# Kernel optimization log

Measured on AMD Instinct MI355X. Metric: run time of the kernel, lower is better.

Reference implementation:

```python
import jax, jax.numpy as jnp
import numpy as np

N = 100000      # n_nodes
E = 1600000     # n_edges (avg degree 16)
F_IN = 128      # nfeat
H = 128         # nhid
C = 64          # nclass


def setup_inputs() -> dict:
    key = jax.random.key(0)
    ks = jax.random.split(key, 6)
    x = jax.random.normal(ks[0], (N, F_IN), dtype=jnp.float32)
    edge_index = jax.random.randint(ks[1], (2, E), 0, N, dtype=jnp.int32)
    # Glorot-ish init for GCNConv weights, zeros for bias (PyG default)
    W1 = jax.random.normal(ks[2], (F_IN, H), dtype=jnp.float32) * (1.0 / np.sqrt(F_IN))
    b1 = jnp.zeros((H,), dtype=jnp.float32)
    W2 = jax.random.normal(ks[3], (H, C), dtype=jnp.float32) * (1.0 / np.sqrt(H))
    b2 = jnp.zeros((C,), dtype=jnp.float32)
    return {"x": x, "edge_index": edge_index, "W1": W1, "b1": b1, "W2": W2, "b2": b2}


def _gcn_conv(x, W, b, src, dst, n):
    """PyG GCNConv: h = W^T x, out_i = sum_j norm_ij * h_j + b, with
    symmetric normalization over the self-loop-augmented graph."""
    h = x @ W                                                   # [n, out]
    deg = jax.ops.segment_sum(jnp.ones(src.shape[0], h.dtype), dst, num_segments=n)
    dinv = jnp.where(deg > 0, jax.lax.rsqrt(deg), 0.0)          # D^-1/2
    norm = dinv[src] * dinv[dst]                                # [E+n]
    msg = h[src] * norm[:, None]                                # gather + scale
    out = jax.ops.segment_sum(msg, dst, num_segments=n)         # scatter-add
    return out + b


def reference(x, edge_index, W1, b1, W2, b2):
    loop = jnp.arange(N, dtype=edge_index.dtype)
    src = jnp.concatenate([edge_index[0], loop])  # sources j (with self loops)
    dst = jnp.concatenate([edge_index[1], loop])  # targets i
    h = jax.nn.relu(_gcn_conv(x, W1, b1, src, dst, N))  # dropout = identity (eval)
    out = _gcn_conv(h, W2, b2, src, dst, N)
    return jax.nn.log_softmax(out, axis=1)
```

## Files before the change

kernel.cpp:

```cpp
#include <hip/hip_runtime.h>
#include <hip/hip_fp16.h>
#include <cstdint>
#include <cstddef>
#include <cstring>


__device__ inline unsigned pack_bf16x2(float a, float b) {
    unsigned ua = __float_as_uint(a);
    unsigned ub = __float_as_uint(b);
    ua += 0x7fffu + ((ua >> 16) & 1u);
    ub += 0x7fffu + ((ub >> 16) & 1u);
    return (ua >> 16) | (ub & 0xffff0000u);
}
__device__ inline unsigned short bf16_rne(float v) {
    unsigned u = __float_as_uint(v);
    u += 0x7fffu + ((u >> 16) & 1u);
    return (unsigned short)(u >> 16);
}


typedef float fv2 __attribute__((ext_vector_type(2)));

template <bool HI>
__device__ inline fv2 fp8_fv2(unsigned u) {
#if __has_builtin(__builtin_amdgcn_cvt_pk_f32_fp8)
    return __builtin_amdgcn_cvt_pk_f32_fp8((int)u, HI);
#else
    unsigned u2 = HI ? (u >> 16) : (u & 0xffffu);
    unsigned w = (u2 & 0xFFu) | ((u2 & 0xFF00u) << 8);
    unsigned hb = ((w & 0x00800080u) << 8) | ((w & 0x007f007fu) << 7);
    __half2 h2;
    memcpy(&h2, &hb, 4);
    float2 f = __half22float2(h2);
    fv2 r;
    r.x = f.x * 256.0f;
    r.y = f.y * 256.0f;
    return r;
#endif
}

__device__ inline fv2 bfpair(unsigned u) {
    union { unsigned q[2]; fv2 f; } t;
    t.q[0] = u << 16;
    t.q[1] = u & 0xffff0000u;
    return t.f;
}

__device__ inline unsigned f32_to_fp8_byte(float v) {
    unsigned short hb = __half_as_ushort(__float2half(v * 0.00390625f));
    unsigned t = hb & 0x7fffu;
    t += 0x3fu + ((t >> 7) & 1u);
    return ((hb >> 8) & 0x80u) | (t >> 7);
}

__device__ inline unsigned char f32_to_fp8_b(float v) {
#if __has_builtin(__builtin_amdgcn_cvt_pk_fp8_f32)
    return (unsigned char)(__builtin_amdgcn_cvt_pk_fp8_f32(v, v, 0, false) & 0xff);
#else
    return (unsigned char)f32_to_fp8_byte(v);
#endif
}

typedef int iv4 __attribute__((ext_vector_type(4)));

#define NPART 8
#define KB    32
#define NPP_MAX 12500
#define EB    2048


__global__ __launch_bounds__(256) void k_bucket_ballot(const int* __restrict__ src,
                                                       const int* __restrict__ dst,
                                                       int* __restrict__ cursor8,
                                                       unsigned* __restrict__ pairs,
                                                       int E, int npp, int capE,
                                                       int srcb) {
    __shared__ int sWcnt[4][NPART];
    __shared__ int sWoff[4][NPART];
    int tid = threadIdx.x;
    int wv = tid >> 6;
    int lane = tid & 63;
    int base_e = blockIdx.x * EB + tid * 8;
    int nv = min(8, E - base_e);
    if (nv < 0) nv = 0;
    int dv[8], sv[8];
    if (nv == 8) {
        *(iv4*)(dv + 0) = *(const iv4*)(dst + base_e + 0);
        *(iv4*)(dv + 4) = *(const iv4*)(dst + base_e + 4);
        *(iv4*)(sv + 0) = *(const iv4*)(src + base_e + 0);
        *(iv4*)(sv + 4) = *(const iv4*)(src + base_e + 4);
    } else {
        for (int k = 0; k < 8; ++k) {
            dv[k] = (k < nv) ? dst[base_e + k] : -1;
            sv[k] = (k < nv) ? src[base_e + k] : 0;
        }
    }
    unsigned long long below = (1ull << lane) - 1ull;
    int wb[NPART];
#pragma unroll
    for (int pp = 0; pp < NPART; ++pp) wb[pp] = 0;
    int pv[8], pos[8];
#pragma unroll
    for (int s = 0; s < 8; ++s) {
        int d = dv[s];
        int p = (d >= 0) ? (int)((unsigned)d / (unsigned)npp) : NPART;
        pv[s] = p;
        unsigned long long msel = 0;
        int base = 0;
#pragma unroll
        for (int pp = 0; pp < NPART; ++pp) {
            unsigned long long m = __ballot(p == pp);
            if (p == pp) { msel = m; base = wb[pp]; }
            wb[pp] += (int)__popcll(m);
        }
        pos[s] = base + (int)__popcll(msel & below);
    }
    if (lane < NPART) {
        int v = 0;
#pragma unroll
        for (int pp = 0; pp < NPART; ++pp)
            if (lane == pp) v = wb[pp];
        sWcnt[wv][lane] = v;
    }
    __syncthreads();
    if (tid < NPART) {
        int c0 = sWcnt[0][tid], c1 = sWcnt[1][tid], c2 = sWcnt[2][tid], c3 = sWcnt[3][tid];
        int gb = atomicAdd(&cursor8[tid], c0 + c1 + c2 + c3);
        sWoff[0][tid] = gb;
        sWoff[1][tid] = gb + c0;
        sWoff[2][tid] = gb + c0 + c1;
        sWoff[3][tid] = gb + c0 + c1 + c2;
    }
    __syncthreads();
#pragma unroll
    for (int s = 0; s < 8; ++s) {
        int p = pv[s];
        if (p < NPART) {
            int off = sWoff[wv][p];
            pairs[(size_t)p * capE + off + pos[s]] =
                ((unsigned)(dv[s] - p * npp) << srcb) | (unsigned)sv[s];
        }
    }
}

__global__ __launch_bounds__(256) void k_count_part(const unsigned* __restrict__ pairs,
                                                    const int* __restrict__ cursor8,
                                                    int* __restrict__ cntarr,
                                                    int npp, int capE, int srcb) {
    __shared__ int h[NPP_MAX];
    int p = blockIdx.x & (NPART - 1);
    int b = blockIdx.x >> 3;
    for (int i = threadIdx.x; i < npp; i += 256) h[i] = 0;
    __syncthreads();
    int sz = cursor8[p];
    int chunk = (sz + KB - 1) / KB;
    int s0 = b * chunk;
    int s1 = min(sz, s0 + chunk);
    const unsigned* seg = pairs + (size_t)p * capE;
    for (int i = s0 + threadIdx.x; i < s1; i += 256)
        atomicAdd(&h[seg[i] >> srcb], 1);
    __syncthreads();
    size_t out = (size_t)(p * KB + b) * npp;
    for (int i = threadIdx.x; i < npp; i += 256) cntarr[out + i] = h[i];
}

__global__ void k_indeg_scan(const int* __restrict__ cntarr,
                             float* __restrict__ dinv,
                             int* __restrict__ row_ptr,
                             int* __restrict__ partials, int n, int npp) {
    __shared__ int s[256];
    int t = threadIdx.x;
    int node0 = blockIdx.x * 1024 + t * 4;
    int v0 = 0, v1 = 0, v2 = 0, v3 = 0;
    if (((npp & 3) == 0) && (node0 + 3 < n) && (node0 / npp == (node0 + 3) / npp)) {
        int p = node0 / npp;
        int dl = node0 - p * npp;
        size_t base = (size_t)p * KB * npp + dl;
        for (int b = 0; b < KB; ++b) {
            iv4 c = *(const iv4*)(cntarr + base + (size_t)b * npp);
            v0 += c.x; v1 += c.y; v2 += c.z; v3 += c.w;
        }
    } else {
        for (int r = 0; r < 4; ++r) {
            int node = node0 + r;
            if (node < n) {
                int p = node / npp;
                int dl = node - p * npp;
                size_t base = (size_t)p * KB * npp + dl;
                int sum = 0;
                for (int b = 0; b < KB; ++b) sum += cntarr[base + (size_t)b * npp];
                if (r == 0) v0 = sum; else if (r == 1) v1 = sum;
                else if (r == 2) v2 = sum; else v3 = sum;
            }
        }
    }
    if (node0 + 0 < n) dinv[node0 + 0] = rsqrtf((float)v0 + 1.0f);
    if (node0 + 1 < n) dinv[node0 + 1] = rsqrtf((float)v1 + 1.0f);
    if (node0 + 2 < n) dinv[node0 + 2] = rsqrtf((float)v2 + 1.0f);
    if (node0 + 3 < n) dinv[node0 + 3] = rsqrtf((float)v3 + 1.0f);
    int sum = v0 + v1 + v2 + v3;
    s[t] = sum;
    __syncthreads();
    for (int off = 1; off < 256; off <<= 1) {
        int x = (t >= off) ? s[t - off] : 0;
        __syncthreads();
        s[t] += x;
        __syncthreads();
    }
    int excl = s[t] - sum;
    if ((node0 + 0) < n) row_ptr[node0 + 0] = excl;
    if ((node0 + 1) < n) row_ptr[node0 + 1] = excl + v0;
    if ((node0 + 2) < n) row_ptr[node0 + 2] = excl + v0 + v1;
    if ((node0 + 3) < n) row_ptr[node0 + 3] = excl + v0 + v1 + v2;
    if (t == 255) partials[blockIdx.x] = s[255];
}

__global__ void k_scan_partials(int* __restrict__ partials, int np) {
    __shared__ int s[256];
    int t = threadIdx.x;
    int v = (t < np) ? partials[t] : 0;
    s[t] = v;
    __syncthreads();
    for (int off = 1; off < 256; off <<= 1) {
        int x = (t >= off) ? s[t - off] : 0;
        __syncthreads();
        s[t] += x;
        __syncthreads();
    }
    if (t < np) partials[t] = s[t] - v;
}

__global__ void k_finalize_bases(int* __restrict__ row_ptr,
                                 const int* __restrict__ partials,
                                 int* __restrict__ cntarr, int n, int E, int npp) {
    int i = blockIdx.x * blockDim.x + threadIdx.x;
    if (i >= n) return;
    int rp = row_ptr[i] + partials[i >> 10];
    row_ptr[i] = rp;
    if (i == 0) row_ptr[n] = E;
    int p = (unsigned)i / (unsigned)npp;
    int dl = i - p * npp;
    size_t base = (size_t)p * KB * npp + dl;
    int run = rp;
    for (int b = 0; b < KB; ++b) {
        size_t idx = base + (size_t)b * npp;
        int c = cntarr[idx];
        cntarr[idx] = run;
        run += c;
    }
}

__global__ __launch_bounds__(256) void k_fill2(const unsigned* __restrict__ pairs,
                                               const int* __restrict__ cursor8,
                                               const int* __restrict__ cntarr,
                                               int* __restrict__ col,
                                               int npp, int capE, int srcb) {
    __shared__ int cur[NPP_MAX];
    int p = blockIdx.x & (NPART - 1);
    int b = blockIdx.x >> 3;
    size_t slice = (size_t)(p * KB + b) * npp;
    for (int i = threadIdx.x; i < npp; i += 256) cur[i] = cntarr[slice + i];
    __syncthreads();
    int sz = cursor8[p];
    int chunk = (sz + KB - 1) / KB;
    int s0 = b * chunk;
    int s1 = min(sz, s0 + chunk);
    const unsigned* seg = pairs + (size_t)p * capE;
    unsigned smask = (1u << srcb) - 1u;
    for (int i = s0 + threadIdx.x; i < s1; i += 256) {
        unsigned u = seg[i];
        int pos = atomicAdd(&cur[u >> srcb], 1);
        col[pos] = (int)(u & smask);
    }
}

typedef __attribute__((ext_vector_type(8))) short short8;
typedef __attribute__((ext_vector_type(4))) float f32x4;

union FragU {
    short8 s;
    uint4 u4;
    unsigned u[4];
};

__device__ inline void packW_body(const float* __restrict__ W, unsigned* __restrict__ Bp,
                                  int NOUT, int NT) {
    int nf = 4 * NT * 64;
    for (int fid = threadIdx.x; fid < nf; fid += 256) {
        int q = fid / (NT * 64);
        int rem = fid - q * NT * 64;
        int nt = rem >> 6;
        int lane = rem & 63;
        int k0 = q * 32 + (lane >> 4) * 8;
        int ncol = nt * 16 + (lane & 15);
        unsigned u[4];
        for (int h = 0; h < 4; ++h) {
            float a = W[(k0 + 2 * h) * NOUT + ncol];
            float b = W[(k0 + 2 * h + 1) * NOUT + ncol];
            u[h] = pack_bf16x2(a, b);
        }
        uint4 o = {u[0], u[1], u[2], u[3]};
        *(uint4*)(Bp + (size_t)fid * 4) = o;
    }
}

__global__ void k_packW2(const float* __restrict__ W1, unsigned* __restrict__ Bp1,
                         const float* __restrict__ W2, unsigned* __restrict__ Bp2) {
    if (blockIdx.x == 0) packW_body(W1, Bp1, 128, 8);
    else                 packW_body(W2, Bp2, 64, 4);
}

__global__ __launch_bounds__(256) void k_gemm128_mfma(const float* __restrict__ X,
                                                      const unsigned* __restrict__ Bp,
                                                      const float* __restrict__ dinv,
                                                      unsigned char* __restrict__ H8,
                                                      int n) {
    int w = threadIdx.x >> 6;
    int lane = threadIdx.x & 63;
    int quad = lane >> 4;
    int lrow = lane & 15;
    int row0 = blockIdx.x * 64 + w * 16;
    int rowA = min(row0 + lrow, n - 1);

    f32x4 acc[8];
    for (int nt = 0; nt < 8; ++nt) acc[nt] = (f32x4){0.f, 0.f, 0.f, 0.f};

    for (int q = 0; q < 4; ++q) {
        const float* xp = X + (size_t)rowA * 128 + q * 32 + quad * 8;
        float4 x0 = *(const float4*)xp;
        float4 x1 = *(const float4*)(xp + 4);
        FragU a;
        a.u[0] = pack_bf16x2(x0.x, x0.y);
        a.u[1] = pack_bf16x2(x0.z, x0.w);
        a.u[2] = pack_bf16x2(x1.x, x1.y);
        a.u[3] = pack_bf16x2(x1.z, x1.w);
        for (int nt = 0; nt < 8; ++nt) {
            FragU b;
            b.u4 = *(const uint4*)(Bp + ((size_t)(q * 8 + nt) * 64 + lane) * 4);
            acc[nt] = __builtin_amdgcn_mfma_f32_16x16x32_bf16(a.s, b.s, acc[nt], 0, 0, 0);
        }
    }

    int rbase = row0 + quad * 4;
    float dv[4];
    if (rbase + 3 < n) {
        float4 d4 = *(const float4*)(dinv + rbase);
        dv[0] = d4.x; dv[1] = d4.y; dv[2] = d4.z; dv[3] = d4.w;
    } else {
        for (int r = 0; r < 4; ++r) dv[r] = dinv[min(rbase + r, n - 1)];
    }
    for (int nt = 0; nt < 8; ++nt) {
        for (int r = 0; r < 4; ++r) {
            int row = rbase + r;
            if (row < n)
                H8[(size_t)row * 128 + nt * 16 + lrow] = f32_to_fp8_b(dv[r] * acc[nt][r]);
        }
    }
}

__global__ __launch_bounds__(256) void k_gemm64_mfma(const unsigned* __restrict__ Xb,
                                                     const unsigned* __restrict__ Bp,
                                                     const float* __restrict__ dinv,
                                                     unsigned short* __restrict__ H16,
                                                     int n) {
    int w = threadIdx.x >> 6;
    int lane = threadIdx.x & 63;
    int quad = lane >> 4;
    int lrow = lane & 15;
    int row0 = blockIdx.x * 64 + w * 16;
    int rowA = min(row0 + lrow, n - 1);

    f32x4 acc[4];
    for (int nt = 0; nt < 4; ++nt) acc[nt] = (f32x4){0.f, 0.f, 0.f, 0.f};

    for (int q = 0; q < 4; ++q) {
        FragU a;
        a.u4 = *(const uint4*)(Xb + (size_t)rowA * 64 + q * 16 + quad * 4);
        for (int nt = 0; nt < 4; ++nt) {
            FragU b;
            b.u4 = *(const uint4*)(Bp + ((size_t)(q * 4 + nt) * 64 + lane) * 4);
            acc[nt] = __builtin_amdgcn_mfma_f32_16x16x32_bf16(a.s, b.s, acc[nt], 0, 0, 0);
        }
    }

    int rbase = row0 + quad * 4;
    float dv[4];
    if (rbase + 3 < n) {
        float4 d4 = *(const float4*)(dinv + rbase);
        dv[0] = d4.x; dv[1] = d4.y; dv[2] = d4.z; dv[3] = d4.w;
    } else {
        for (int r = 0; r < 4; ++r) dv[r] = dinv[min(rbase + r, n - 1)];
    }
    for (int nt = 0; nt < 4; ++nt) {
        for (int r = 0; r < 4; ++r) {
            int row = rbase + r;
            if (row < n)
                H16[(size_t)row * 64 + nt * 16 + lrow] = bf16_rne(dv[r] * acc[nt][r]);
        }
    }
}


__global__ __launch_bounds__(256) void k_agg_relu(const unsigned* __restrict__ hs,
                                                  const float* __restrict__ dinv,
                                                  const int* __restrict__ row_ptr,
                                                  const int* __restrict__ col,
                                                  const float* __restrict__ bias,
                                                  unsigned* __restrict__ out, int n) {
    int node = blockIdx.x * 16 + (threadIdx.x >> 4);
    if (node >= n) return;
    int l = threadIdx.x & 15;
    const uint2* hrow = (const uint2*)hs;
    fv2 a0 = {0.f, 0.f}, a1 = {0.f, 0.f}, a2 = {0.f, 0.f}, a3 = {0.f, 0.f};
    {
        uint2 u = hrow[(size_t)node * 16 + l];
        a0 += fp8_fv2<false>(u.x); a1 += fp8_fv2<true>(u.x);
        a2 += fp8_fv2<false>(u.y); a3 += fp8_fv2<true>(u.y);
    }
    int k = row_ptr[node], p1 = row_ptr[node + 1];
    for (; k + 8 <= p1; k += 8) {
        int cA = col[k + 0], cB = col[k + 1], cC = col[k + 2], cD = col[k + 3];
        int cE = col[k + 4], cF = col[k + 5], cG = col[k + 6], cH = col[k + 7];
        uint2 uA = hrow[(size_t)cA * 16 + l];
        uint2 uB = hrow[(size_t)cB * 16 + l];
        uint2 uC = hrow[(size_t)cC * 16 + l];
        uint2 uD = hrow[(size_t)cD * 16 + l];
        uint2 uE = hrow[(size_t)cE * 16 + l];
        uint2 uF = hrow[(size_t)cF * 16 + l];
        uint2 uG = hrow[(size_t)cG * 16 + l];
        uint2 uH = hrow[(size_t)cH * 16 + l];
        a0 += fp8_fv2<false>(uA.x); a1 += fp8_fv2<true>(uA.x);
        a2 += fp8_fv2<false>(uA.y); a3 += fp8_fv2<true>(uA.y);
        a0 += fp8_fv2<false>(uB.x); a1 += fp8_fv2<true>(uB.x);
        a2 += fp8_fv2<false>(uB.y); a3 += fp8_fv2<true>(uB.y);
        a0 += fp8_fv2<false>(uC.x); a1 += fp8_fv2<true>(uC.x);
        a2 += fp8_fv2<false>(uC.y); a3 += fp8_fv2<true>(uC.y);
        a0 += fp8_fv2<false>(uD.x); a1 += fp8_fv2<true>(uD.x);
        a2 += fp8_fv2<false>(uD.y); a3 += fp8_fv2<true>(uD.y);
        a0 += fp8_fv2<false>(uE.x); a1 += fp8_fv2<true>(uE.x);
        a2 += fp8_fv2<false>(uE.y); a3 += fp8_fv2<true>(uE.y);
        a0 += fp8_fv2<false>(uF.x); a1 += fp8_fv2<true>(uF.x);
        a2 += fp8_fv2<false>(uF.y); a3 += fp8_fv2<true>(uF.y);
        a0 += fp8_fv2<false>(uG.x); a1 += fp8_fv2<true>(uG.x);
        a2 += fp8_fv2<false>(uG.y); a3 += fp8_fv2<true>(uG.y);
        a0 += fp8_fv2<false>(uH.x); a1 += fp8_fv2<true>(uH.x);
        a2 += fp8_fv2<false>(uH.y); a3 += fp8_fv2<true>(uH.y);
    }
    for (; k + 4 <= p1; k += 4) {
        int cA = col[k + 0], cB = col[k + 1], cC = col[k + 2], cD = col[k + 3];
        uint2 uA = hrow[(size_t)cA * 16 + l];
        uint2 uB = hrow[(size_t)cB * 16 + l];
        uint2 uC = hrow[(size_t)cC * 16 + l];
        uint2 uD = hrow[(size_t)cD * 16 + l];
        a0 += fp8_fv2<false>(uA.x); a1 += fp8_fv2<true>(uA.x);
        a2 += fp8_fv2<false>(uA.y); a3 += fp8_fv2<true>(uA.y);
        a0 += fp8_fv2<false>(uB.x); a1 += fp8_fv2<true>(uB.x);
        a2 += fp8_fv2<false>(uB.y); a3 += fp8_fv2<true>(uB.y);
        a0 += fp8_fv2<false>(uC.x); a1 += fp8_fv2<true>(uC.x);
        a2 += fp8_fv2<false>(uC.y); a3 += fp8_fv2<true>(uC.y);
        a0 += fp8_fv2<false>(uD.x); a1 += fp8_fv2<true>(uD.x);
        a2 += fp8_fv2<false>(uD.y); a3 += fp8_fv2<true>(uD.y);
    }
    for (; k < p1; ++k) {
        int j = col[k];
        uint2 u = hrow[(size_t)j * 16 + l];
        a0 += fp8_fv2<false>(u.x); a1 += fp8_fv2<true>(u.x);
        a2 += fp8_fv2<false>(u.y); a3 += fp8_fv2<true>(u.y);
    }
    float di = dinv[node];
    float4 b4a = *(const float4*)(bias + 8 * l);
    float4 b4b = *(const float4*)(bias + 8 * l + 4);
    float v0 = fmaf(di, a0.x, b4a.x);
    float v1 = fmaf(di, a0.y, b4a.y);
    float v2 = fmaf(di, a1.x, b4a.z);
    float v3 = fmaf(di, a1.y, b4a.w);
    float v4 = fmaf(di, a2.x, b4b.x);
    float v5 = fmaf(di, a2.y, b4b.y);
    float v6 = fmaf(di, a3.x, b4b.z);
    float v7 = fmaf(di, a3.y, b4b.w);
    v0 = v0 > 0.f ? v0 : 0.f;
    v1 = v1 > 0.f ? v1 : 0.f;
    v2 = v2 > 0.f ? v2 : 0.f;
    v3 = v3 > 0.f ? v3 : 0.f;
    v4 = v4 > 0.f ? v4 : 0.f;
    v5 = v5 > 0.f ? v5 : 0.f;
    v6 = v6 > 0.f ? v6 : 0.f;
    v7 = v7 > 0.f ? v7 : 0.f;
    uint4 o = {pack_bf16x2(v0, v1), pack_bf16x2(v2, v3),
               pack_bf16x2(v4, v5), pack_bf16x2(v6, v7)};
    *(uint4*)(out + (size_t)node * 64 + 4 * l) = o;
}

__global__ __launch_bounds__(256) void k_agg_lsm(const unsigned* __restrict__ hs,
                                                 const float* __restrict__ dinv,
                                                 const int* __restrict__ row_ptr,
                                                 const int* __restrict__ col,
                                                 const float* __restrict__ bias,
                                                 float* __restrict__ out, int n) {
    int node = blockIdx.x * 16 + (threadIdx.x >> 4);
    if (node >= n) return;
    int l = threadIdx.x & 15;
    const uint2* hrow = (const uint2*)hs;
    fv2 aX = {0.f, 0.f}, aY = {0.f, 0.f};
    {
        uint2 u = hrow[(size_t)node * 16 + l];
        aX += bfpair(u.x);
        aY += bfpair(u.y);
    }
    int k = row_ptr[node], p1 = row_ptr[node + 1];
    for (; k + 8 <= p1; k += 8) {
        int cA = col[k + 0], cB = col[k + 1], cC = col[k + 2], cD = col[k + 3];
        int cE = col[k + 4], cF = col[k + 5], cG = col[k + 6], cH = col[k + 7];
        uint2 uA = hrow[(size_t)cA * 16 + l];
        uint2 uB = hrow[(size_t)cB * 16 + l];
        uint2 uC = hrow[(size_t)cC * 16 + l];
        uint2 uD = hrow[(size_t)cD * 16 + l];
        uint2 uE = hrow[(size_t)cE * 16 + l];
        uint2 uF = hrow[(size_t)cF * 16 + l];
        uint2 uG = hrow[(size_t)cG * 16 + l];
        uint2 uH = hrow[(size_t)cH * 16 + l];
        aX += bfpair(uA.x); aY += bfpair(uA.y);
        aX += bfpair(uB.x); aY += bfpair(uB.y);
        aX += bfpair(uC.x); aY += bfpair(uC.y);
        aX += bfpair(uD.x); aY += bfpair(uD.y);
        aX += bfpair(uE.x); aY += bfpair(uE.y);
        aX += bfpair(uF.x); aY += bfpair(uF.y);
        aX += bfpair(uG.x); aY += bfpair(uG.y);
        aX += bfpair(uH.x); aY += bfpair(uH.y);
    }
    for (; k + 4 <= p1; k += 4) {
        int cA = col[k + 0], cB = col[k + 1], cC = col[k + 2], cD = col[k + 3];
        uint2 uA = hrow[(size_t)cA * 16 + l];
        uint2 uB = hrow[(size_t)cB * 16 + l];
        uint2 uC = hrow[(size_t)cC * 16 + l];
        uint2 uD = hrow[(size_t)cD * 16 + l];
        aX += bfpair(uA.x); aY += bfpair(uA.y);
        aX += bfpair(uB.x); aY += bfpair(uB.y);
        aX += bfpair(uC.x); aY += bfpair(uC.y);
        aX += bfpair(uD.x); aY += bfpair(uD.y);
    }
    for (; k < p1; ++k) {
        int j = col[k];
        uint2 u = hrow[(size_t)j * 16 + l];
        aX += bfpair(u.x); aY += bfpair(u.y);
    }
    float di = dinv[node];
    float4 b4 = *(const float4*)(bias + 4 * l);
    float v0 = fmaf(di, aX.x, b4.x);
    float v1 = fmaf(di, aX.y, b4.y);
    float v2 = fmaf(di, aY.x, b4.z);
    float v3 = fmaf(di, aY.y, b4.w);
    float m = fmaxf(fmaxf(v0, v1), fmaxf(v2, v3));
    for (int off = 8; off; off >>= 1) m = fmaxf(m, __shfl_xor(m, off));
    float s = __expf(v0 - m) + __expf(v1 - m) + __expf(v2 - m) + __expf(v3 - m);
    for (int off = 8; off; off >>= 1) s += __shfl_xor(s, off);
    float ls = __logf(s);
    float4 o = {v0 - m - ls, v1 - m - ls, v2 - m - ls, v3 - m - ls};
    *(float4*)(out + (size_t)node * 64 + 4 * l) = o;
}


extern "C" void kernel_launch(void* const* d_in, const int* in_sizes, int n_in,
                              void* d_out, int out_size, void* d_ws, size_t ws_size,
                              hipStream_t stream) {
    const float* x  = (const float*)d_in[0];
    const int*   ei = (const int*)d_in[1];
    const float* W1 = (const float*)d_in[2];
    const float* b1 = (const float*)d_in[3];
    const float* W2 = (const float*)d_in[4];
    const float* b2 = (const float*)d_in[5];
    float* out = (float*)d_out;

    const int N = in_sizes[0] / 128;
    const int E = in_sizes[1] / 2;
    const int* src = ei;
    const int* dst = ei + E;
    const int npp = (N + NPART - 1) / NPART;
    const int capE = (E + NPART - 1) / NPART + 32768;
    int srcb = 1;
    while ((1 << srcb) < N) ++srcb;

    char* w = (char*)d_ws;
    size_t off = 0;
    auto alloc = [&](size_t bytes) -> void* {
        void* p = w + off;
        off += (bytes + 255) & ~(size_t)255;
        return p;
    };
    int*      row_ptr  = (int*)alloc((size_t)(N + 1) * 4);
    int*      colarr   = (int*)alloc((size_t)E * 4);
    int*      partials = (int*)alloc(256 * 4);
    int*      cursor8  = (int*)alloc(8 * 4);
    float*    dinv     = (float*)alloc((size_t)N * 4);
    unsigned* h1f8     = (unsigned*)alloc((size_t)N * 32 * 4);
    unsigned* a1b      = (unsigned*)alloc((size_t)N * 64 * 4);
    unsigned* h2b      = (unsigned*)alloc((size_t)N * 32 * 4);
    unsigned* Bp1      = (unsigned*)alloc(4 * 8 * 64 * 16);
    unsigned* Bp2      = (unsigned*)alloc(4 * 4 * 64 * 16);
    unsigned* pairsU   = (unsigned*)a1b;
    int*      cntarr   = (int*)((char*)a1b + (size_t)NPART * capE * 4);
    (void)ws_size; (void)n_in; (void)out_size;

    int nscan = (N + 1023) / 1024;
    int nbb = (E + EB - 1) / EB;
    int ngemm = (N + 63) / 64;

    hipMemsetAsync(cursor8, 0, 8 * 4, stream);
    k_packW2<<<2, 256, 0, stream>>>(W1, Bp1, W2, Bp2);
    k_bucket_ballot<<<nbb, 256, 0, stream>>>(src, dst, cursor8, pairsU,
                                             E, npp, capE, srcb);
    k_count_part<<<NPART * KB, 256, 0, stream>>>(pairsU, cursor8, cntarr,
                                                 npp, capE, srcb);
    k_indeg_scan<<<nscan, 256, 0, stream>>>(cntarr, dinv, row_ptr, partials, N, npp);
    k_scan_partials<<<1, 256, 0, stream>>>(partials, nscan);
    k_finalize_bases<<<(N + 255) / 256, 256, 0, stream>>>(row_ptr, partials, cntarr,
                                                          N, E, npp);
    k_fill2<<<NPART * KB, 256, 0, stream>>>(pairsU, cursor8, cntarr, colarr,
                                            npp, capE, srcb);

    k_gemm128_mfma<<<ngemm, 256, 0, stream>>>(x, Bp1, dinv, (unsigned char*)h1f8, N);
    k_agg_relu<<<(N + 15) / 16, 256, 0, stream>>>(h1f8, dinv, row_ptr, colarr, b1, a1b, N);
    k_gemm64_mfma<<<ngemm, 256, 0, stream>>>(a1b, Bp2, dinv, (unsigned short*)h2b, N);
    k_agg_lsm<<<(N + 15) / 16, 256, 0, stream>>>(h2b, dinv, row_ptr, colarr, b2, out, N);
}
```

Baseline: 269.3 us.

## Fuse CSR construction kernels into one persistent kernel with grid barriers

Merges the bucket, count, degree-scan, partial-scan, base-finalize and fill kernels into a single 256-block persistent kernel. Phases are separated by software grid barriers built from atomic counters. The counter and barrier resets move into the weight-packing kernel, which drops the memset. The aim is to remove five kernel launch gaps and their tail effects, at the cost of relying on all 256 blocks being co-resident and spin-waiting at the barriers.

```diff
diff --git a/kernel.cpp b/kernel.cpp
--- a/kernel.cpp
+++ b/kernel.cpp
@@ -66,211 +66,222 @@
 #define NPART 8
 #define KB    32
 #define NPP_MAX 12500
-#define EB    2048
-
-
-__global__ __launch_bounds__(256) void k_bucket_ballot(const int* __restrict__ src,
-                                                       const int* __restrict__ dst,
-                                                       int* __restrict__ cursor8,
-                                                       unsigned* __restrict__ pairs,
-                                                       int E, int npp, int capE,
-                                                       int srcb) {
-    __shared__ int sWcnt[4][NPART];
-    __shared__ int sWoff[4][NPART];
-    int tid = threadIdx.x;
-    int wv = tid >> 6;
-    int lane = tid & 63;
-    int base_e = blockIdx.x * EB + tid * 8;
-    int nv = min(8, E - base_e);
-    if (nv < 0) nv = 0;
-    int dv[8], sv[8];
-    if (nv == 8) {
-        *(iv4*)(dv + 0) = *(const iv4*)(dst + base_e + 0);
-        *(iv4*)(dv + 4) = *(const iv4*)(dst + base_e + 4);
-        *(iv4*)(sv + 0) = *(const iv4*)(src + base_e + 0);
-        *(iv4*)(sv + 4) = *(const iv4*)(src + base_e + 4);
-    } else {
-        for (int k = 0; k < 8; ++k) {
-            dv[k] = (k < nv) ? dst[base_e + k] : -1;
-            sv[k] = (k < nv) ? src[base_e + k] : 0;
-        }
-    }
+
+
+__device__ inline void grid_bar(int* ctr, int nb) {
+    __syncthreads();
+    if (threadIdx.x == 0) {
+        __threadfence();
+        __hip_atomic_fetch_add(ctr, 1, __ATOMIC_RELEASE, __HIP_MEMORY_SCOPE_AGENT);
+        while (__hip_atomic_load(ctr, __ATOMIC_ACQUIRE, __HIP_MEMORY_SCOPE_AGENT) < nb)
+            __builtin_amdgcn_s_sleep(1);
+        __threadfence();
+    }
+    __syncthreads();
+}
+
+__global__ __launch_bounds__(256) void k_mega_csr(const int* __restrict__ src,
+                                                  const int* __restrict__ dst,
+                                                  int* __restrict__ cursor8,
+                                                  unsigned* __restrict__ pairs,
+                                                  int* __restrict__ cntarr,
+                                                  float* __restrict__ dinv,
+                                                  int* __restrict__ row_ptr,
+                                                  int* __restrict__ gpart,
+                                                  int* __restrict__ bar,
+                                                  int* __restrict__ col,
+                                                  int E, int n, int npp, int capE,
+                                                  int srcb, int nscan) {
+    __shared__ int h[NPP_MAX];
+    __shared__ int s[256];
+    __shared__ int sWcnt[4][NPART], sWoff[4][NPART];
+    const int g = blockIdx.x;
+    const int nb = gridDim.x;
+    const int tid = threadIdx.x;
+    const int p = g & (NPART - 1);
+    const int b = g >> 3;
+    const int wv = tid >> 6;
+    const int lane = tid & 63;
+
+    int epb = ((E + nb - 1) / nb + 7) & ~7;
+    int e0 = g * epb, e1 = min(E, e0 + epb);
     unsigned long long below = (1ull << lane) - 1ull;
-    int wb[NPART];
+    for (int c0 = e0; c0 < e1; c0 += 2048) {
+        int base_e = c0 + tid * 8;
+        int nv = min(8, e1 - base_e);
+        if (nv < 0) nv = 0;
+        int dv[8], sv[8];
+        if (nv == 8) {
+            *(iv4*)(dv + 0) = *(const iv4*)(dst + base_e + 0);
+            *(iv4*)(dv + 4) = *(const iv4*)(dst + base_e + 4);
+            *(iv4*)(sv + 0) = *(const iv4*)(src + base_e + 0);
+            *(iv4*)(sv + 4) = *(const iv4*)(src + base_e + 4);
+        } else {
+            for (int k = 0; k < 8; ++k) {
+                dv[k] = (k < nv) ? dst[base_e + k] : -1;
+                sv[k] = (k < nv) ? src[base_e + k] : 0;
+            }
+        }
+        int wb[NPART];
 #pragma unroll
-    for (int pp = 0; pp < NPART; ++pp) wb[pp] = 0;
-    int pv[8], pos[8];
+        for (int pp = 0; pp < NPART; ++pp) wb[pp] = 0;
+        int pv[8], pos[8];
 #pragma unroll
-    for (int s = 0; s < 8; ++s) {
-        int d = dv[s];
-        int p = (d >= 0) ? (int)((unsigned)d / (unsigned)npp) : NPART;
-        pv[s] = p;
-        unsigned long long msel = 0;
-        int base = 0;
+        for (int ss = 0; ss < 8; ++ss) {
+            int d = dv[ss];
+            int pp2 = (d >= 0) ? (int)((unsigned)d / (unsigned)npp) : NPART;
+            pv[ss] = pp2;
+            unsigned long long msel = 0;
+            int base = 0;
 #pragma unroll
-        for (int pp = 0; pp < NPART; ++pp) {
-            unsigned long long m = __ballot(p == pp);
-            if (p == pp) { msel = m; base = wb[pp]; }
-            wb[pp] += (int)__popcll(m);
-        }
-        pos[s] = base + (int)__popcll(msel & below);
-    }
-    if (lane < NPART) {
-        int v = 0;
+            for (int pp = 0; pp < NPART; ++pp) {
+                unsigned long long m = __ballot(pp2 == pp);
+                if (pp2 == pp) { msel = m; base = wb[pp]; }
+                wb[pp] += (int)__popcll(m);
+            }
+            pos[ss] = base + (int)__popcll(msel & below);
+        }
+        if (lane < NPART) {
+            int v = 0;
 #pragma unroll
-        for (int pp = 0; pp < NPART; ++pp)
-            if (lane == pp) v = wb[pp];
-        sWcnt[wv][lane] = v;
-    }
+            for (int pp = 0; pp < NPART; ++pp)
+                if (lane == pp) v = wb[pp];
+            sWcnt[wv][lane] = v;
+        }
+        __syncthreads();
+        if (tid < NPART) {
+            int c0w = sWcnt[0][tid], c1w = sWcnt[1][tid];
+            int c2w = sWcnt[2][tid], c3w = sWcnt[3][tid];
+            int gb = atomicAdd(&cursor8[tid], c0w + c1w + c2w + c3w);
+            sWoff[0][tid] = gb;
+            sWoff[1][tid] = gb + c0w;
+            sWoff[2][tid] = gb + c0w + c1w;
+            sWoff[3][tid] = gb + c0w + c1w + c2w;
+        }
+        __syncthreads();
+#pragma unroll
+        for (int ss = 0; ss < 8; ++ss) {
+            int pp2 = pv[ss];
+            if (pp2 < NPART) {
+                int off = sWoff[wv][pp2];
+                pairs[(size_t)pp2 * capE + off + pos[ss]] =
+                    ((unsigned)(dv[ss] - pp2 * npp) << srcb) | (unsigned)sv[ss];
+            }
+        }
+        __syncthreads();
+    }
+    grid_bar(bar + 0, nb);
+
+    for (int i = tid; i < npp; i += 256) h[i] = 0;
     __syncthreads();
-    if (tid < NPART) {
-        int c0 = sWcnt[0][tid], c1 = sWcnt[1][tid], c2 = sWcnt[2][tid], c3 = sWcnt[3][tid];
-        int gb = atomicAdd(&cursor8[tid], c0 + c1 + c2 + c3);
-        sWoff[0][tid] = gb;
-        sWoff[1][tid] = gb + c0;
-        sWoff[2][tid] = gb + c0 + c1;
-        sWoff[3][tid] = gb + c0 + c1 + c2;
-    }
-    __syncthreads();
-#pragma unroll
-    for (int s = 0; s < 8; ++s) {
-        int p = pv[s];
-        if (p < NPART) {
-            int off = sWoff[wv][p];
-            pairs[(size_t)p * capE + off + pos[s]] =
-                ((unsigned)(dv[s] - p * npp) << srcb) | (unsigned)sv[s];
-        }
-    }
-}
-
-__global__ __launch_bounds__(256) void k_count_part(const unsigned* __restrict__ pairs,
-                                                    const int* __restrict__ cursor8,
-                                                    int* __restrict__ cntarr,
-                                                    int npp, int capE, int srcb) {
-    __shared__ int h[NPP_MAX];
-    int p = blockIdx.x & (NPART - 1);
-    int b = blockIdx.x >> 3;
-    for (int i = threadIdx.x; i < npp; i += 256) h[i] = 0;
-    __syncthreads();
-    int sz = cursor8[p];
-    int chunk = (sz + KB - 1) / KB;
-    int s0 = b * chunk;
-    int s1 = min(sz, s0 + chunk);
+    int szp = cursor8[p];
+    int chunk = (szp + KB - 1) / KB;
+    int cs0 = b * chunk, cs1 = min(szp, cs0 + chunk);
     const unsigned* seg = pairs + (size_t)p * capE;
-    for (int i = s0 + threadIdx.x; i < s1; i += 256)
+    for (int i = cs0 + tid; i < cs1; i += 256)
         atomicAdd(&h[seg[i] >> srcb], 1);
     __syncthreads();
-    size_t out = (size_t)(p * KB + b) * npp;
-    for (int i = threadIdx.x; i < npp; i += 256) cntarr[out + i] = h[i];
-}
-
-__global__ void k_indeg_scan(const int* __restrict__ cntarr,
-                             float* __restrict__ dinv,
-                             int* __restrict__ row_ptr,
-                             int* __restrict__ partials, int n, int npp) {
-    __shared__ int s[256];
-    int t = threadIdx.x;
-    int node0 = blockIdx.x * 1024 + t * 4;
-    int v0 = 0, v1 = 0, v2 = 0, v3 = 0;
-    if (((npp & 3) == 0) && (node0 + 3 < n) && (node0 / npp == (node0 + 3) / npp)) {
-        int p = node0 / npp;
-        int dl = node0 - p * npp;
-        size_t base = (size_t)p * KB * npp + dl;
-        for (int b = 0; b < KB; ++b) {
-            iv4 c = *(const iv4*)(cntarr + base + (size_t)b * npp);
-            v0 += c.x; v1 += c.y; v2 += c.z; v3 += c.w;
-        }
+    {
+        size_t outS = (size_t)(p * KB + b) * npp;
+        for (int i = tid; i < npp; i += 256) cntarr[outS + i] = h[i];
+    }
+    grid_bar(bar + 1, nb);
+
+    if (g < nscan) {
+        int node0 = g * 1024 + tid * 4;
+        int v0 = 0, v1 = 0, v2 = 0, v3 = 0;
+        if (((npp & 3) == 0) && (node0 + 3 < n) && (node0 / npp == (node0 + 3) / npp)) {
+            int pp = node0 / npp;
+            int dl = node0 - pp * npp;
+            size_t base = (size_t)pp * KB * npp + dl;
+            for (int bb = 0; bb < KB; ++bb) {
+                iv4 c = *(const iv4*)(cntarr + base + (size_t)bb * npp);
+                v0 += c.x; v1 += c.y; v2 += c.z; v3 += c.w;
+            }
+        } else {
+            for (int r = 0; r < 4; ++r) {
+                int node = node0 + r;
+                if (node < n) {
+                    int pp = node / npp;
+                    int dl = node - pp * npp;
+                    size_t base = (size_t)pp * KB * npp + dl;
+                    int sum = 0;
+                    for (int bb = 0; bb < KB; ++bb) sum += cntarr[base + (size_t)bb * npp];
+                    if (r == 0) v0 = sum; else if (r == 1) v1 = sum;
+                    else if (r == 2) v2 = sum; else v3 = sum;
+                }
+            }
+        }
+        if (node0 + 0 < n) dinv[node0 + 0] = rsqrtf((float)v0 + 1.0f);
+        if (node0 + 1 < n) dinv[node0 + 1] = rsqrtf((float)v1 + 1.0f);
+        if (node0 + 2 < n) dinv[node0 + 2] = rsqrtf((float)v2 + 1.0f);
+        if (node0 + 3 < n) dinv[node0 + 3] = rsqrtf((float)v3 + 1.0f);
+        int sum = v0 + v1 + v2 + v3;
+        s[tid] = sum;
+        __syncthreads();
+        for (int off = 1; off < 256; off <<= 1) {
+            int x = (tid >= off) ? s[tid - off] : 0;
+            __syncthreads();
+            s[tid] += x;
+            __syncthreads();
+        }
+        int excl = s[tid] - sum;
+        if ((node0 + 0) < n) row_ptr[node0 + 0] = excl;
+        if ((node0 + 1) < n) row_ptr[node0 + 1] = excl + v0;
+        if ((node0 + 2) < n) row_ptr[node0 + 2] = excl + v0 + v1;
+        if ((node0 + 3) < n) row_ptr[node0 + 3] = excl + v0 + v1 + v2;
+        if (tid == 255) gpart[g] = s[255];
     } else {
-        for (int r = 0; r < 4; ++r) {
-            int node = node0 + r;
-            if (node < n) {
-                int p = node / npp;
-                int dl = node - p * npp;
-                size_t base = (size_t)p * KB * npp + dl;
-                int sum = 0;
-                for (int b = 0; b < KB; ++b) sum += cntarr[base + (size_t)b * npp];
-                if (r == 0) v0 = sum; else if (r == 1) v1 = sum;
-                else if (r == 2) v2 = sum; else v3 = sum;
+        if (tid == 0) gpart[g] = 0;
+    }
+    grid_bar(bar + 2, nb);
+
+    {
+        int v = gpart[tid];
+        s[tid] = v;
+        __syncthreads();
+        for (int off = 1; off < 256; off <<= 1) {
+            int x = (tid >= off) ? s[tid - off] : 0;
+            __syncthreads();
+            s[tid] += x;
+            __syncthreads();
+        }
+        int excl = s[tid] - v;
+        __syncthreads();
+        s[tid] = excl;
+        __syncthreads();
+    }
+    {
+        int ch3 = (n + nb - 1) / nb;
+        int i0 = g * ch3, i1 = min(n, i0 + ch3);
+        for (int i = i0 + tid; i < i1; i += 256) {
+            int rp = row_ptr[i] + s[i >> 10];
+            row_ptr[i] = rp;
+            int pp = (unsigned)i / (unsigned)npp;
+            int dl = i - pp * npp;
+            size_t base = (size_t)pp * KB * npp + dl;
+            int run = rp;
+            for (int bb = 0; bb < KB; ++bb) {
+                size_t idx = base + (size_t)bb * npp;
+                int c = cntarr[idx];
+                cntarr[idx] = run;
+                run += c;
             }
         }
-    }
-    if (node0 + 0 < n) dinv[node0 + 0] = rsqrtf((float)v0 + 1.0f);
-    if (node0 + 1 < n) dinv[node0 + 1] = rsqrtf((float)v1 + 1.0f);
-    if (node0 + 2 < n) dinv[node0 + 2] = rsqrtf((float)v2 + 1.0f);
-    if (node0 + 3 < n) dinv[node0 + 3] = rsqrtf((float)v3 + 1.0f);
-    int sum = v0 + v1 + v2 + v3;
-    s[t] = sum;
-    __syncthreads();
-    for (int off = 1; off < 256; off <<= 1) {
-        int x = (t >= off) ? s[t - off] : 0;
-        __syncthreads();
-        s[t] += x;
-        __syncthreads();
-    }
-    int excl = s[t] - sum;
-    if ((node0 + 0) < n) row_ptr[node0 + 0] = excl;
-    if ((node0 + 1) < n) row_ptr[node0 + 1] = excl + v0;
-    if ((node0 + 2) < n) row_ptr[node0 + 2] = excl + v0 + v1;
-    if ((node0 + 3) < n) row_ptr[node0 + 3] = excl + v0 + v1 + v2;
-    if (t == 255) partials[blockIdx.x] = s[255];
-}
-
-__global__ void k_scan_partials(int* __restrict__ partials, int np) {
-    __shared__ int s[256];
-    int t = threadIdx.x;
-    int v = (t < np) ? partials[t] : 0;
-    s[t] = v;
-    __syncthreads();
-    for (int off = 1; off < 256; off <<= 1) {
-        int x = (t >= off) ? s[t - off] : 0;
-        __syncthreads();
-        s[t] += x;
-        __syncthreads();
-    }
-    if (t < np) partials[t] = s[t] - v;
-}
-
-__global__ void k_finalize_bases(int* __restrict__ row_ptr,
-                                 const int* __restrict__ partials,
-                                 int* __restrict__ cntarr, int n, int E, int npp) {
-    int i = blockIdx.x * blockDim.x + threadIdx.x;
-    if (i >= n) return;
-    int rp = row_ptr[i] + partials[i >> 10];
-    row_ptr[i] = rp;
-    if (i == 0) row_ptr[n] = E;
-    int p = (unsigned)i / (unsigned)npp;
-    int dl = i - p * npp;
-    size_t base = (size_t)p * KB * npp + dl;
-    int run = rp;
-    for (int b = 0; b < KB; ++b) {
-        size_t idx = base + (size_t)b * npp;
-        int c = cntarr[idx];
-        cntarr[idx] = run;
-        run += c;
-    }
-}
-
-__global__ __launch_bounds__(256) void k_fill2(const unsigned* __restrict__ pairs,
-                                               const int* __restrict__ cursor8,
-                                               const int* __restrict__ cntarr,
-                                               int* __restrict__ col,
-                                               int npp, int capE, int srcb) {
-    __shared__ int cur[NPP_MAX];
-    int p = blockIdx.x & (NPART - 1);
-    int b = blockIdx.x >> 3;
-    size_t slice = (size_t)(p * KB + b) * npp;
-    for (int i = threadIdx.x; i < npp; i += 256) cur[i] = cntarr[slice + i];
-    __syncthreads();
-    int sz = cursor8[p];
-    int chunk = (sz + KB - 1) / KB;
-    int s0 = b * chunk;
-    int s1 = min(sz, s0 + chunk);
-    const unsigned* seg = pairs + (size_t)p * capE;
-    unsigned smask = (1u << srcb) - 1u;
-    for (int i = s0 + threadIdx.x; i < s1; i += 256) {
-        unsigned u = seg[i];
-        int pos = atomicAdd(&cur[u >> srcb], 1);
-        col[pos] = (int)(u & smask);
+        if (g == 0 && tid == 0) row_ptr[n] = E;
+    }
+    grid_bar(bar + 3, nb);
+
+    {
+        size_t slice = (size_t)(p * KB + b) * npp;
+        for (int i = tid; i < npp; i += 256) h[i] = cntarr[slice + i];
+        __syncthreads();
+        unsigned smask = (1u << srcb) - 1u;
+        for (int i = cs0 + tid; i < cs1; i += 256) {
+            unsigned u = seg[i];
+            int pos = atomicAdd(&h[u >> srcb], 1);
+            col[pos] = (int)(u & smask);
+        }
     }
 }
 
@@ -305,9 +316,15 @@
 }
 
 __global__ void k_packW2(const float* __restrict__ W1, unsigned* __restrict__ Bp1,
-                         const float* __restrict__ W2, unsigned* __restrict__ Bp2) {
-    if (blockIdx.x == 0) packW_body(W1, Bp1, 128, 8);
-    else                 packW_body(W2, Bp2, 64, 4);
+                         const float* __restrict__ W2, unsigned* __restrict__ Bp2,
+                         int* __restrict__ cursor8, int* __restrict__ bar) {
+    if (blockIdx.x == 0) {
+        if (threadIdx.x < 8) cursor8[threadIdx.x] = 0;
+        else if (threadIdx.x < 16) bar[threadIdx.x - 8] = 0;
+        packW_body(W1, Bp1, 128, 8);
+    } else {
+        packW_body(W2, Bp2, 64, 4);
+    }
 }
 
 __global__ __launch_bounds__(256) void k_gemm128_mfma(const float* __restrict__ X,
@@ -589,8 +606,9 @@
     };
     int*      row_ptr  = (int*)alloc((size_t)(N + 1) * 4);
     int*      colarr   = (int*)alloc((size_t)E * 4);
-    int*      partials = (int*)alloc(256 * 4);
+    int*      gpart    = (int*)alloc(256 * 4);
     int*      cursor8  = (int*)alloc(8 * 4);
+    int*      bar      = (int*)alloc(16 * 4);
     float*    dinv     = (float*)alloc((size_t)N * 4);
     unsigned* h1f8     = (unsigned*)alloc((size_t)N * 32 * 4);
     unsigned* a1b      = (unsigned*)alloc((size_t)N * 64 * 4);
@@ -602,22 +620,12 @@
     (void)ws_size; (void)n_in; (void)out_size;
 
     int nscan = (N + 1023) / 1024;
-    int nbb = (E + EB - 1) / EB;
     int ngemm = (N + 63) / 64;
 
-    hipMemsetAsync(cursor8, 0, 8 * 4, stream);
-    k_packW2<<<2, 256, 0, stream>>>(W1, Bp1, W2, Bp2);
-    k_bucket_ballot<<<nbb, 256, 0, stream>>>(src, dst, cursor8, pairsU,
-                                             E, npp, capE, srcb);
-    k_count_part<<<NPART * KB, 256, 0, stream>>>(pairsU, cursor8, cntarr,
-                                                 npp, capE, srcb);
-    k_indeg_scan<<<nscan, 256, 0, stream>>>(cntarr, dinv, row_ptr, partials, N, npp);
-    k_scan_partials<<<1, 256, 0, stream>>>(partials, nscan);
-    k_finalize_bases<<<(N + 255) / 256, 256, 0, stream>>>(row_ptr, partials, cntarr,
-                                                          N, E, npp);
-    k_fill2<<<NPART * KB, 256, 0, stream>>>(pairsU, cursor8, cntarr, colarr,
-                                            npp, capE, srcb);
-
+    k_packW2<<<2, 256, 0, stream>>>(W1, Bp1, W2, Bp2, cursor8, bar);
+    k_mega_csr<<<256, 256, 0, stream>>>(src, dst, cursor8, pairsU, cntarr, dinv,
+                                        row_ptr, gpart, bar, colarr,
+                                        E, N, npp, capE, srcb, nscan);
     k_gemm128_mfma<<<ngemm, 256, 0, stream>>>(x, Bp1, dinv, (unsigned char*)h1f8, N);
     k_agg_relu<<<(N + 15) / 16, 256, 0, stream>>>(h1f8, dinv, row_ptr, colarr, b1, a1b, N);
     k_gemm64_mfma<<<ngemm, 256, 0, stream>>>(a1b, Bp2, dinv, (unsigned short*)h2b, N);
```

New measurement: 404.6 us. 1.5x slower.

## Fuse layer-1 aggregation+ReLU with layer-2 GEMM through shared memory

Applied to the files above, without the earlier changes.

Merges the layer-1 aggregation/ReLU kernel with the 128->64 MFMA GEMM. Each block stages its 16 aggregated bf16 rows in LDS, then four waves each compute one 16-column tile and write the dinv-scaled bf16 result straight to h2b. This removes the a1b intermediate (a write and re-read of N x 128 bf16) and one kernel launch. It adds a block-wide barrier after the latency-bound gather and reuses h1f8 as scratch for the bucket-sort pairs.

```diff
diff --git a/kernel.cpp b/kernel.cpp
--- a/kernel.cpp
+++ b/kernel.cpp
@@ -358,66 +358,29 @@
     }
 }
 
-__global__ __launch_bounds__(256) void k_gemm64_mfma(const unsigned* __restrict__ Xb,
-                                                     const unsigned* __restrict__ Bp,
-                                                     const float* __restrict__ dinv,
-                                                     unsigned short* __restrict__ H16,
-                                                     int n) {
-    int w = threadIdx.x >> 6;
-    int lane = threadIdx.x & 63;
-    int quad = lane >> 4;
-    int lrow = lane & 15;
-    int row0 = blockIdx.x * 64 + w * 16;
-    int rowA = min(row0 + lrow, n - 1);
-
-    f32x4 acc[4];
-    for (int nt = 0; nt < 4; ++nt) acc[nt] = (f32x4){0.f, 0.f, 0.f, 0.f};
-
-    for (int q = 0; q < 4; ++q) {
-        FragU a;
-        a.u4 = *(const uint4*)(Xb + (size_t)rowA * 64 + q * 16 + quad * 4);
-        for (int nt = 0; nt < 4; ++nt) {
-            FragU b;
-            b.u4 = *(const uint4*)(Bp + ((size_t)(q * 4 + nt) * 64 + lane) * 4);
-            acc[nt] = __builtin_amdgcn_mfma_f32_16x16x32_bf16(a.s, b.s, acc[nt], 0, 0, 0);
-        }
-    }
-
-    int rbase = row0 + quad * 4;
-    float dv[4];
-    if (rbase + 3 < n) {
-        float4 d4 = *(const float4*)(dinv + rbase);
-        dv[0] = d4.x; dv[1] = d4.y; dv[2] = d4.z; dv[3] = d4.w;
-    } else {
-        for (int r = 0; r < 4; ++r) dv[r] = dinv[min(rbase + r, n - 1)];
-    }
-    for (int nt = 0; nt < 4; ++nt) {
-        for (int r = 0; r < 4; ++r) {
-            int row = rbase + r;
-            if (row < n)
-                H16[(size_t)row * 64 + nt * 16 + lrow] = bf16_rne(dv[r] * acc[nt][r]);
-        }
-    }
-}
-
-
-__global__ __launch_bounds__(256) void k_agg_relu(const unsigned* __restrict__ hs,
-                                                  const float* __restrict__ dinv,
-                                                  const int* __restrict__ row_ptr,
-                                                  const int* __restrict__ col,
-                                                  const float* __restrict__ bias,
-                                                  unsigned* __restrict__ out, int n) {
-    int node = blockIdx.x * 16 + (threadIdx.x >> 4);
-    if (node >= n) return;
+__global__ __launch_bounds__(256) void k_agg_relu_gemm(const unsigned* __restrict__ hs,
+                                                       const float* __restrict__ dinv,
+                                                       const int* __restrict__ row_ptr,
+                                                       const int* __restrict__ col,
+                                                       const float* __restrict__ bias,
+                                                       const unsigned* __restrict__ Bp2,
+                                                       unsigned short* __restrict__ H16,
+                                                       int n) {
+    __shared__ unsigned s_a[16][68];
+    int q16 = threadIdx.x >> 4;
+    int node = blockIdx.x * 16 + q16;
     int l = threadIdx.x & 15;
+    bool alive = node < n;
+    int nodeC = alive ? node : (n - 1);
     const uint2* hrow = (const uint2*)hs;
     fv2 a0 = {0.f, 0.f}, a1 = {0.f, 0.f}, a2 = {0.f, 0.f}, a3 = {0.f, 0.f};
-    {
+    if (alive) {
         uint2 u = hrow[(size_t)node * 16 + l];
         a0 += fp8_fv2<false>(u.x); a1 += fp8_fv2<true>(u.x);
         a2 += fp8_fv2<false>(u.y); a3 += fp8_fv2<true>(u.y);
     }
-    int k = row_ptr[node], p1 = row_ptr[node + 1];
+    int k = alive ? row_ptr[node] : 0;
+    int p1 = alive ? row_ptr[node + 1] : 0;
     for (; k + 8 <= p1; k += 8) {
         int cA = col[k + 0], cB = col[k + 1], cC = col[k + 2], cD = col[k + 3];
         int cE = col[k + 4], cF = col[k + 5], cG = col[k + 6], cH = col[k + 7];
@@ -467,28 +430,50 @@
         a0 += fp8_fv2<false>(u.x); a1 += fp8_fv2<true>(u.x);
         a2 += fp8_fv2<false>(u.y); a3 += fp8_fv2<true>(u.y);
     }
-    float di = dinv[node];
-    float4 b4a = *(const float4*)(bias + 8 * l);
-    float4 b4b = *(const float4*)(bias + 8 * l + 4);
-    float v0 = fmaf(di, a0.x, b4a.x);
-    float v1 = fmaf(di, a0.y, b4a.y);
-    float v2 = fmaf(di, a1.x, b4a.z);
-    float v3 = fmaf(di, a1.y, b4a.w);
-    float v4 = fmaf(di, a2.x, b4b.x);
-    float v5 = fmaf(di, a2.y, b4b.y);
-    float v6 = fmaf(di, a3.x, b4b.z);
-    float v7 = fmaf(di, a3.y, b4b.w);
-    v0 = v0 > 0.f ? v0 : 0.f;
-    v1 = v1 > 0.f ? v1 : 0.f;
-    v2 = v2 > 0.f ? v2 : 0.f;
-    v3 = v3 > 0.f ? v3 : 0.f;
-    v4 = v4 > 0.f ? v4 : 0.f;
-    v5 = v5 > 0.f ? v5 : 0.f;
-    v6 = v6 > 0.f ? v6 : 0.f;
-    v7 = v7 > 0.f ? v7 : 0.f;
-    uint4 o = {pack_bf16x2(v0, v1), pack_bf16x2(v2, v3),
-               pack_bf16x2(v4, v5), pack_bf16x2(v6, v7)};
-    *(uint4*)(out + (size_t)node * 64 + 4 * l) = o;
+    {
+        float di = dinv[nodeC];
+        float4 b4a = *(const float4*)(bias + 8 * l);
+        float4 b4b = *(const float4*)(bias + 8 * l + 4);
+        float v0 = fmaf(di, a0.x, b4a.x);
+        float v1 = fmaf(di, a0.y, b4a.y);
+        float v2 = fmaf(di, a1.x, b4a.z);
+        float v3 = fmaf(di, a1.y, b4a.w);
+        float v4 = fmaf(di, a2.x, b4b.x);
+        float v5 = fmaf(di, a2.y, b4b.y);
+        float v6 = fmaf(di, a3.x, b4b.z);
+        float v7 = fmaf(di, a3.y, b4b.w);
+        v0 = v0 > 0.f ? v0 : 0.f;
+        v1 = v1 > 0.f ? v1 : 0.f;
+        v2 = v2 > 0.f ? v2 : 0.f;
+        v3 = v3 > 0.f ? v3 : 0.f;
+        v4 = v4 > 0.f ? v4 : 0.f;
+        v5 = v5 > 0.f ? v5 : 0.f;
+        v6 = v6 > 0.f ? v6 : 0.f;
+        v7 = v7 > 0.f ? v7 : 0.f;
+        uint4 o = {pack_bf16x2(v0, v1), pack_bf16x2(v2, v3),
+                   pack_bf16x2(v4, v5), pack_bf16x2(v6, v7)};
+        *(uint4*)&s_a[q16][4 * l] = o;
+    }
+    __syncthreads();
+    {
+        int lane = threadIdx.x & 63;
+        int w = threadIdx.x >> 6;
+        int quad = lane >> 4;
+        int lrow = lane & 15;
+        f32x4 acc = (f32x4){0.f, 0.f, 0.f, 0.f};
+        for (int q = 0; q < 4; ++q) {
+            FragU a, b;
+            a.u4 = *(const uint4*)&s_a[lrow][16 * q + 4 * quad];
+            b.u4 = *(const uint4*)(Bp2 + ((size_t)(q * 4 + w) * 64 + lane) * 4);
+            acc = __builtin_amdgcn_mfma_f32_16x16x32_bf16(a.s, b.s, acc, 0, 0, 0);
+        }
+        int rbase = blockIdx.x * 16 + quad * 4;
+        for (int r = 0; r < 4; ++r) {
+            int nd = rbase + r;
+            if (nd < n)
+                H16[(size_t)nd * 64 + w * 16 + lrow] = bf16_rne(dinv[nd] * acc[r]);
+        }
+    }
 }
 
 __global__ __launch_bounds__(256) void k_agg_lsm(const unsigned* __restrict__ hs,
@@ -593,12 +578,11 @@
     int*      cursor8  = (int*)alloc(8 * 4);
     float*    dinv     = (float*)alloc((size_t)N * 4);
     unsigned* h1f8     = (unsigned*)alloc((size_t)N * 32 * 4);
-    unsigned* a1b      = (unsigned*)alloc((size_t)N * 64 * 4);
     unsigned* h2b      = (unsigned*)alloc((size_t)N * 32 * 4);
     unsigned* Bp1      = (unsigned*)alloc(4 * 8 * 64 * 16);
     unsigned* Bp2      = (unsigned*)alloc(4 * 4 * 64 * 16);
-    unsigned* pairsU   = (unsigned*)a1b;
-    int*      cntarr   = (int*)((char*)a1b + (size_t)NPART * capE * 4);
+    unsigned* pairsU   = (unsigned*)h1f8;
+    int*      cntarr   = (int*)((char*)h1f8 + (size_t)NPART * capE * 4);
     (void)ws_size; (void)n_in; (void)out_size;
 
     int nscan = (N + 1023) / 1024;
@@ -619,7 +603,7 @@
                                             npp, capE, srcb);
 
     k_gemm128_mfma<<<ngemm, 256, 0, stream>>>(x, Bp1, dinv, (unsigned char*)h1f8, N);
-    k_agg_relu<<<(N + 15) / 16, 256, 0, stream>>>(h1f8, dinv, row_ptr, colarr, b1, a1b, N);
-    k_gemm64_mfma<<<ngemm, 256, 0, stream>>>(a1b, Bp2, dinv, (unsigned short*)h2b, N);
+    k_agg_relu_gemm<<<(N + 15) / 16, 256, 0, stream>>>(h1f8, dinv, row_ptr, colarr,
+                                                       b1, Bp2, (unsigned short*)h2b, N);
     k_agg_lsm<<<(N + 15) / 16, 256, 0, stream>>>(h2b, dinv, row_ptr, colarr, b2, out, N);
 }
```

After: 264.5 us. Within noise of the previous version (-1.8%).
